# Optimization experiments

Measured on AMD Instinct MI355X. Metric: run time of the kernel, lower is better.

## Reference

```python
import jax, jax.numpy as jnp
import numpy as np

NEG_SLOPE = 0.2

def gat_conv(x, edge_index, W, a_src, a_dst, bias, heads, channels):
    # PyG GATConv (add_self_loops=False, dropout off in eval)
    N = x.shape[0]
    h = (x @ W).reshape(N, heads, channels)               # [N,H,C]
    src, dst = edge_index[0], edge_index[1]
    e_src = jnp.einsum('nhc,hc->nh', h, a_src)            # [N,H]
    e_dst = jnp.einsum('nhc,hc->nh', h, a_dst)
    e = jax.nn.leaky_relu(e_src[src] + e_dst[dst], NEG_SLOPE)  # [E,H]
    # softmax over incoming edges of each destination node
    m = jax.ops.segment_max(e, dst, num_segments=N)       # [N,H]
    ex = jnp.exp(e - m[dst])
    s = jax.ops.segment_sum(ex, dst, num_segments=N)
    alpha = ex / (s[dst] + 1e-16)                         # [E,H]
    msg = h[src] * alpha[:, :, None]                      # [E,H,C]
    out = jax.ops.segment_sum(msg, dst, num_segments=N)   # [N,H,C]
    return out.reshape(N, heads * channels) + bias


def setup_inputs() -> dict:
    key = jax.random.key(0)
    ks = jax.random.split(key, 12)
    N, E, SED, HID, H, F_OUT = 20000, 320000, 768, 128, 4, 128
    return {
        'x': jax.random.normal(ks[0], (N, SED), jnp.float32),
        'edge_index': jax.random.randint(ks[1], (2, E), 0, N, jnp.int32),
        'sentence_embedding': jax.random.normal(ks[2], (SED,), jnp.float32),
        'W1': jax.random.normal(ks[3], (2 * SED, H * HID), jnp.float32) * 0.02,
        'a1_src': jax.random.normal(ks[4], (H, HID), jnp.float32) * 0.1,
        'a1_dst': jax.random.normal(ks[5], (H, HID), jnp.float32) * 0.1,
        'b1': jax.random.normal(ks[6], (H * HID,), jnp.float32) * 0.02,
        'W2': jax.random.normal(ks[7], (H * HID, F_OUT), jnp.float32) * 0.02,
        'a2_src': jax.random.normal(ks[8], (1, F_OUT), jnp.float32) * 0.1,
        'a2_dst': jax.random.normal(ks[9], (1, F_OUT), jnp.float32) * 0.1,
        'b2': jax.random.normal(ks[10], (F_OUT,), jnp.float32) * 0.02,
    }


def reference(x, edge_index, sentence_embedding, W1, a1_src, a1_dst, b1, W2, a2_src, a2_dst, b2):
    N = x.shape[0]
    sent = jnp.broadcast_to(sentence_embedding[None, :], (N, sentence_embedding.shape[0]))
    h = jnp.concatenate([x, sent], axis=1)                # [N, 2*SED]
    h = gat_conv(h, edge_index, W1, a1_src, a1_dst, b1, heads=4, channels=128)
    h = jax.nn.elu(h)
    out = gat_conv(h, edge_index, W2, a2_src, a2_dst, b2, heads=1, channels=128)
    return out
```

## Files before the change

kernel.cpp:

```cpp
#include <hip/hip_runtime.h>
#include <cstdint>
#include <cstddef>

#define NSLOPE 0.2f
#define CAP 96

typedef __attribute__((ext_vector_type(8))) short bf16x8;
typedef __attribute__((ext_vector_type(4))) float f32x4;
typedef __attribute__((ext_vector_type(2))) float f32x2;
typedef unsigned short ushort_t;

__device__ inline ushort_t f2bf(float f) {
    union { float f; unsigned u; } v; v.f = f;
    unsigned u = v.u;
    unsigned r = (u + 0x7fffu + ((u >> 16) & 1u)) >> 16;
    return (ushort_t)r;
}
__device__ inline f32x2 unpack2(unsigned u) {
    union { unsigned u; float f; } lo, hi;
    lo.u = u << 16;
    hi.u = u & 0xffff0000u;
    f32x2 r; r.x = lo.f; r.y = hi.f;
    return r;
}
__device__ inline float leaky(float v) { return (v > 0.f) ? v : NSLOPE * v; }
__device__ inline float sel4(float4 q, bool b1, bool b2) {
    return b2 ? (b1 ? q.w : q.z) : (b1 ? q.y : q.x);
}

__global__ __launch_bounds__(256) void prep_scatter_kernel(
    const float* __restrict__ x, ushort_t* __restrict__ x_bf16, size_t nx,
    const float* __restrict__ W1, ushort_t* __restrict__ W1T,
    const float* __restrict__ W2, ushort_t* __restrict__ W2T,
    const float* __restrict__ sent, float* __restrict__ svec,
    const int* __restrict__ ei, int E,
    int* __restrict__ cnt, int* __restrict__ bucket, int nbCast)
{
    __shared__ float tile[32][33];
    int bid = blockIdx.x;
    int tid = threadIdx.x;
    if (bid < 384) {
        int k0 = (bid % 24) * 32, n0 = (bid / 24) * 32;
        int tx = tid & 31, ty = tid >> 5;
#pragma unroll
        for (int i = 0; i < 4; ++i)
            tile[ty + i * 8][tx] = W1[(size_t)(k0 + ty + i * 8) * 512 + n0 + tx];
        __syncthreads();
#pragma unroll
        for (int i = 0; i < 4; ++i)
            W1T[(size_t)(n0 + ty + i * 8) * 768 + k0 + tx] = f2bf(tile[tx][ty + i * 8]);
        return;
    }
    bid -= 384;
    if (bid < 64) {
        int k0 = (bid % 16) * 32, n0 = (bid / 16) * 32;
        int tx = tid & 31, ty = tid >> 5;
#pragma unroll
        for (int i = 0; i < 4; ++i)
            tile[ty + i * 8][tx] = W2[(size_t)(k0 + ty + i * 8) * 128 + n0 + tx];
        __syncthreads();
#pragma unroll
        for (int i = 0; i < 4; ++i)
            W2T[(size_t)(n0 + ty + i * 8) * 512 + k0 + tx] = f2bf(tile[tx][ty + i * 8]);
        return;
    }
    bid -= 64;
    if (bid < 32) {
        int cb = bid & 1, kb = bid >> 1;
        int c = cb * 256 + tid;
        int k0 = kb * 48;
        float acc = 0.f;
#pragma unroll 8
        for (int k = k0; k < k0 + 48; ++k)
            acc += sent[k] * W1[(size_t)(768 + k) * 512 + c];
        atomicAdd(&svec[c], acc);
        return;
    }
    bid -= 32;
    if (bid < nbCast) {
        size_t i = ((size_t)bid * 256 + tid) * 8;
        if (i < nx) {
            float4 v0 = *(const float4*)(x + i);
            float4 v1 = *(const float4*)(x + i + 4);
            ushort_t r[8] = { f2bf(v0.x), f2bf(v0.y), f2bf(v0.z), f2bf(v0.w),
                              f2bf(v1.x), f2bf(v1.y), f2bf(v1.z), f2bf(v1.w) };
            *(uint4*)(x_bf16 + i) = *(uint4*)r;
        }
        return;
    }
    bid -= nbCast;
    {
        int e = bid * 256 + tid;
        if (e < E) {
            int d = ei[E + e];
            int slot = atomicAdd(&cnt[d], 1);
            if (slot < CAP) bucket[d * CAP + slot] = ei[e];
        }
    }
}

__device__ inline void async_copy16(const void* g, void* l) {
    __builtin_amdgcn_global_load_lds(
        (const __attribute__((address_space(1))) unsigned int*)g,
        (__attribute__((address_space(3))) unsigned int*)l, 16, 0, 0);
}

__global__ __launch_bounds__(256) void mfma_gemm_kernel(
    const ushort_t* __restrict__ A,
    const ushort_t* __restrict__ BT,
    const float* __restrict__ bias,
    ushort_t* __restrict__ Cb,
    const float* __restrict__ asrc,
    const float* __restrict__ adst,
    float* __restrict__ e_src,
    float* __restrict__ e_dst,
    int eStride,
    int M, int K, int Nc)
{
    __shared__ __align__(16) ushort_t lA[4][64 * 32];
    __shared__ __align__(16) ushort_t lB[4][128 * 32];
    __shared__ float e_lds[64][2][2];
    const int tid = threadIdx.x;
    const int wave = tid >> 6;
    const int lane = tid & 63;

    const int hh = blockIdx.y * gridDim.x + blockIdx.x;
    const int xcd = hh & 7;
    const int slot = hh >> 3;
    const int by = xcd + 8 * (slot / gridDim.x);
    const int bx = slot % gridDim.x;

    const int col0 = bx * 128;
    const int row0 = by * 64;
    const int wm = (wave & 1) * 32;
    const int wn = (wave >> 1) * 64;
    const int q = lane >> 4;
    const int ml = lane & 15;

    f32x4 acc[2][4] = {};

    const int rA = tid >> 2;
    const int gA = (tid & 3) ^ ((rA >> 1) & 3);
    int rowS[2], gS[2];
#pragma unroll
    for (int i = 0; i < 2; ++i) {
        int p = wave * 128 + i * 64 + lane;
        int r = p >> 2, s = p & 3;
        rowS[i] = r;
        gS[i] = s ^ ((r >> 1) & 3);
    }

    auto stage = [&](int k0, int buf) {
        {
            int ga = min(row0 + rA, M - 1);
            async_copy16(A + (size_t)ga * K + k0 + gA * 8,
                         &lA[buf][(size_t)(wave * 64) * 8]);
        }
#pragma unroll
        for (int i = 0; i < 2; ++i) {
            int pbs = wave * 128 + i * 64;
            async_copy16(BT + (size_t)(col0 + rowS[i]) * K + k0 + gS[i] * 8,
                         &lB[buf][(size_t)pbs * 8]);
        }
    };

    const int nt = K >> 5;
    stage(0, 0);
    if (nt > 2) {
        stage(32, 1);
        stage(64, 2);
        asm volatile("s_waitcnt vmcnt(6)\n\ts_barrier" ::: "memory");
    } else if (nt > 1) {
        stage(32, 1);
        asm volatile("s_waitcnt vmcnt(3)\n\ts_barrier" ::: "memory");
    } else {
        asm volatile("s_waitcnt vmcnt(0)\n\ts_barrier" ::: "memory");
    }

    for (int t = 0; t < nt; ++t) {
        const int pb = t & 3;
        if (t + 3 < nt) stage((t + 3) << 5, (t + 3) & 3);
        bf16x8 af[2], bfr[4];
#pragma unroll
        for (int tt = 0; tt < 2; ++tt) {
            int m = wm + tt * 16 + ml;
            af[tt] = *(const bf16x8*)&lA[pb][(size_t)(m * 4 + (q ^ ((m >> 1) & 3))) * 8];
        }
#pragma unroll
        for (int tt = 0; tt < 4; ++tt) {
            int n = wn + tt * 16 + ml;
            bfr[tt] = *(const bf16x8*)&lB[pb][(size_t)(n * 4 + (q ^ ((n >> 1) & 3))) * 8];
        }
#pragma unroll
        for (int tm = 0; tm < 2; ++tm)
#pragma unroll
            for (int tn = 0; tn < 4; ++tn)
                acc[tm][tn] = __builtin_amdgcn_mfma_f32_16x16x32_bf16(
                    af[tm], bfr[tn], acc[tm][tn], 0, 0, 0);
        if (t + 3 < nt)
            asm volatile("s_waitcnt vmcnt(6) lgkmcnt(0)\n\ts_barrier" ::: "memory");
        else if (t + 2 < nt)
            asm volatile("s_waitcnt vmcnt(3) lgkmcnt(0)\n\ts_barrier" ::: "memory");
        else if (t + 1 < nt)
            asm volatile("s_waitcnt vmcnt(0) lgkmcnt(0)\n\ts_barrier" ::: "memory");
    }

    float es_acc[2][4] = {};
    float ed_acc[2][4] = {};
#pragma unroll
    for (int tm = 0; tm < 2; ++tm) {
        int rbase = row0 + wm + tm * 16 + q * 4;
#pragma unroll
        for (int tn = 0; tn < 4; ++tn) {
            int col = col0 + wn + tn * 16 + ml;
            float bb = bias ? bias[col] : 0.f;
            float av = asrc[col];
            float dv = adst[col];
#pragma unroll
            for (int r = 0; r < 4; ++r) {
                int row = rbase + r;
                float val = acc[tm][tn][r] + bb;
                if (row < M)
                    Cb[(size_t)row * Nc + col] = f2bf(val);
                es_acc[tm][r] += val * av;
                ed_acc[tm][r] += val * dv;
            }
        }
    }
    const int colhalf = wave >> 1;
#pragma unroll
    for (int tm = 0; tm < 2; ++tm) {
#pragma unroll
        for (int r = 0; r < 4; ++r) {
            float es = es_acc[tm][r], ed2 = ed_acc[tm][r];
#pragma unroll
            for (int st = 1; st < 16; st <<= 1) {
                es += __shfl_xor(es, st);
                ed2 += __shfl_xor(ed2, st);
            }
            if (ml == 0) {
                int rl = wm + tm * 16 + q * 4 + r;
                e_lds[rl][colhalf][0] = es;
                e_lds[rl][colhalf][1] = ed2;
            }
        }
    }
    __syncthreads();
    if (tid < 64) {
        int row = row0 + tid;
        if (row < M) {
            float es = e_lds[tid][0][0] + e_lds[tid][1][0];
            float ed2 = e_lds[tid][0][1] + e_lds[tid][1][1];
            e_src[(size_t)row * eStride + bx] = es;
            e_dst[(size_t)row * eStride + bx] = ed2;
        }
    }
}

__global__ __launch_bounds__(256) void gather1_kernel(
    const ushort_t* __restrict__ h1b, const float* __restrict__ e_src,
    const float* __restrict__ e_dst, const int* __restrict__ cnt,
    const int* __restrict__ bucket, const float* __restrict__ bias,
    ushort_t* __restrict__ outb, int N)
{
    const int lane = threadIdx.x & 63;
    const int wid0 = blockIdx.x * 4 + (threadIdx.x >> 6);
    const int nw = gridDim.x * 4;

    const int h = lane >> 4;
    const bool b1 = (h & 1), b2 = (h & 2);
    const ushort_t* hp = h1b + lane * 8;
    const int c = lane * 8;
    float bias0 = bias[c],     bias1 = bias[c + 1], bias2 = bias[c + 2],
          bias3 = bias[c + 3], bias4 = bias[c + 4], bias5 = bias[c + 5],
          bias6 = bias[c + 6], bias7 = bias[c + 7];

    for (int node = __builtin_amdgcn_readfirstlane(wid0); node < N;
         node = __builtin_amdgcn_readfirstlane(node + nw)) {
        int deg = cnt[node];
        if (deg > CAP) deg = CAP;
        int beg = node * CAP, end = beg + deg;
        float4 ed = *(const float4*)&e_dst[node * 4];
        float edh = sel4(ed, b1, b2);

        f32x2 acc[4] = {};
        float s = 0.f;

        int j = beg;
        const int nb = deg >> 2;

        int4 ia, ib;
        float4 qa0, qa1, qa2, qa3, qb0, qb1, qb2, qb3;
        uint4 ua0, ua1, ua2, ua3, ub0, ub1, ub2, ub3;

        auto load4 = [&](int jj, int4& ix,
                         float4& q0, float4& q1, float4& q2, float4& q3,
                         uint4& u0, uint4& u1, uint4& u2, uint4& u3) {
            ix.x = bucket[jj];     ix.y = bucket[jj + 1];
            ix.z = bucket[jj + 2]; ix.w = bucket[jj + 3];
            q0 = *(const float4*)&e_src[ix.x * 4];
            q1 = *(const float4*)&e_src[ix.y * 4];
            q2 = *(const float4*)&e_src[ix.z * 4];
            q3 = *(const float4*)&e_src[ix.w * 4];
            u0 = *(const uint4*)&hp[(size_t)ix.x * 512];
            u1 = *(const uint4*)&hp[(size_t)ix.y * 512];
            u2 = *(const uint4*)&hp[(size_t)ix.z * 512];
            u3 = *(const uint4*)&hp[(size_t)ix.w * 512];
        };
        auto cons4 = [&](const float4& q0, const float4& q1,
                         const float4& q2, const float4& q3,
                         const uint4& u0, const uint4& u1,
                         const uint4& u2, const uint4& u3) {
            float w0 = __expf(leaky(sel4(q0, b1, b2) + edh));
            float w1 = __expf(leaky(sel4(q1, b1, b2) + edh));
            float w2 = __expf(leaky(sel4(q2, b1, b2) + edh));
            float w3 = __expf(leaky(sel4(q3, b1, b2) + edh));
            s += (w0 + w1) + (w2 + w3);
            f32x2 wv;
            wv.x = w0; wv.y = w0;
            acc[0] += unpack2(u0.x) * wv; acc[1] += unpack2(u0.y) * wv;
            acc[2] += unpack2(u0.z) * wv; acc[3] += unpack2(u0.w) * wv;
            wv.x = w1; wv.y = w1;
            acc[0] += unpack2(u1.x) * wv; acc[1] += unpack2(u1.y) * wv;
            acc[2] += unpack2(u1.z) * wv; acc[3] += unpack2(u1.w) * wv;
            wv.x = w2; wv.y = w2;
            acc[0] += unpack2(u2.x) * wv; acc[1] += unpack2(u2.y) * wv;
            acc[2] += unpack2(u2.z) * wv; acc[3] += unpack2(u2.w) * wv;
            wv.x = w3; wv.y = w3;
            acc[0] += unpack2(u3.x) * wv; acc[1] += unpack2(u3.y) * wv;
            acc[2] += unpack2(u3.z) * wv; acc[3] += unpack2(u3.w) * wv;
        };

        if (nb > 0) {
            load4(j, ia, qa0, qa1, qa2, qa3, ua0, ua1, ua2, ua3); j += 4;
            int b = 1;
            for (; b + 1 < nb; b += 2) {
                load4(j, ib, qb0, qb1, qb2, qb3, ub0, ub1, ub2, ub3); j += 4;
                cons4(qa0, qa1, qa2, qa3, ua0, ua1, ua2, ua3);
                load4(j, ia, qa0, qa1, qa2, qa3, ua0, ua1, ua2, ua3); j += 4;
                cons4(qb0, qb1, qb2, qb3, ub0, ub1, ub2, ub3);
            }
            if (b < nb) {
                load4(j, ib, qb0, qb1, qb2, qb3, ub0, ub1, ub2, ub3); j += 4;
                cons4(qa0, qa1, qa2, qa3, ua0, ua1, ua2, ua3);
                cons4(qb0, qb1, qb2, qb3, ub0, ub1, ub2, ub3);
            } else {
                cons4(qa0, qa1, qa2, qa3, ua0, ua1, ua2, ua3);
            }
        }
        for (; j < end; ++j) {
            int s0 = bucket[j];
            float4 q0 = *(const float4*)&e_src[s0 * 4];
            float w0 = __expf(leaky(sel4(q0, b1, b2) + edh));
            s += w0;
            uint4 u0 = *(const uint4*)&hp[(size_t)s0 * 512];
            f32x2 wv; wv.x = w0; wv.y = w0;
            acc[0] += unpack2(u0.x) * wv; acc[1] += unpack2(u0.y) * wv;
            acc[2] += unpack2(u0.z) * wv; acc[3] += unpack2(u0.w) * wv;
        }
        float rs = 1.f / (s + 1e-16f);
        ushort_t o[8];
        float r0, r1;
        r0 = acc[0].x * rs + bias0; r1 = acc[0].y * rs + bias1;
        r0 = (r0 > 0.f) ? r0 : (__expf(r0) - 1.f);
        r1 = (r1 > 0.f) ? r1 : (__expf(r1) - 1.f);
        o[0] = f2bf(r0); o[1] = f2bf(r1);
        r0 = acc[1].x * rs + bias2; r1 = acc[1].y * rs + bias3;
        r0 = (r0 > 0.f) ? r0 : (__expf(r0) - 1.f);
        r1 = (r1 > 0.f) ? r1 : (__expf(r1) - 1.f);
        o[2] = f2bf(r0); o[3] = f2bf(r1);
        r0 = acc[2].x * rs + bias4; r1 = acc[2].y * rs + bias5;
        r0 = (r0 > 0.f) ? r0 : (__expf(r0) - 1.f);
        r1 = (r1 > 0.f) ? r1 : (__expf(r1) - 1.f);
        o[4] = f2bf(r0); o[5] = f2bf(r1);
        r0 = acc[3].x * rs + bias6; r1 = acc[3].y * rs + bias7;
        r0 = (r0 > 0.f) ? r0 : (__expf(r0) - 1.f);
        r1 = (r1 > 0.f) ? r1 : (__expf(r1) - 1.f);
        o[6] = f2bf(r0); o[7] = f2bf(r1);
        *(uint4*)&outb[(size_t)node * 512 + c] = *(uint4*)o;
    }
}

__global__ __launch_bounds__(256) void gather2_kernel(
    const ushort_t* __restrict__ h2b, const float* __restrict__ e_src,
    const float* __restrict__ e_dst, const int* __restrict__ cnt,
    const int* __restrict__ bucket, const float* __restrict__ bias,
    float* __restrict__ out, int N)
{
    const int lane = threadIdx.x & 63;
    const int wid0 = blockIdx.x * 4 + (threadIdx.x >> 6);
    const int nw = gridDim.x * 4;

    const ushort_t* hp = h2b + lane * 2;
    float biasA = bias[lane * 2], biasB = bias[lane * 2 + 1];

    for (int node = __builtin_amdgcn_readfirstlane(wid0); node < N;
         node = __builtin_amdgcn_readfirstlane(node + nw)) {
        int deg = cnt[node];
        if (deg > CAP) deg = CAP;
        int beg = node * CAP, end = beg + deg;
        float ed = e_dst[node];

        f32x2 acc = { 0.f, 0.f };
        float s = 0.f;

        int j = beg;
        const int nb = deg >> 2;

        int4 ia, ib;
        float fa0, fa1, fa2, fa3, fb0, fb1, fb2, fb3;
        unsigned ua0, ua1, ua2, ua3, ub0, ub1, ub2, ub3;

        auto load4 = [&](int jj, int4& ix,
                         float& f0, float& f1, float& f2, float& f3,
                         unsigned& u0, unsigned& u1, unsigned& u2, unsigned& u3) {
            ix.x = bucket[jj];     ix.y = bucket[jj + 1];
            ix.z = bucket[jj + 2]; ix.w = bucket[jj + 3];
            f0 = e_src[ix.x]; f1 = e_src[ix.y];
            f2 = e_src[ix.z]; f3 = e_src[ix.w];
            u0 = *(const unsigned*)&hp[(size_t)ix.x * 128];
            u1 = *(const unsigned*)&hp[(size_t)ix.y * 128];
            u2 = *(const unsigned*)&hp[(size_t)ix.z * 128];
            u3 = *(const unsigned*)&hp[(size_t)ix.w * 128];
        };
        auto cons4 = [&](float f0, float f1, float f2, float f3,
                         unsigned u0, unsigned u1, unsigned u2, unsigned u3) {
            float w0 = __expf(leaky(f0 + ed));
            float w1 = __expf(leaky(f1 + ed));
            float w2 = __expf(leaky(f2 + ed));
            float w3 = __expf(leaky(f3 + ed));
            s += (w0 + w1) + (w2 + w3);
            f32x2 w0v = { w0, w0 }, w1v = { w1, w1 }, w2v = { w2, w2 }, w3v = { w3, w3 };
            acc += unpack2(u0) * w0v;
            acc += unpack2(u1) * w1v;
            acc += unpack2(u2) * w2v;
            acc += unpack2(u3) * w3v;
        };

        if (nb > 0) {
            load4(j, ia, fa0, fa1, fa2, fa3, ua0, ua1, ua2, ua3); j += 4;
            int b = 1;
            for (; b + 1 < nb; b += 2) {
                load4(j, ib, fb0, fb1, fb2, fb3, ub0, ub1, ub2, ub3); j += 4;
                cons4(fa0, fa1, fa2, fa3, ua0, ua1, ua2, ua3);
                load4(j, ia, fa0, fa1, fa2, fa3, ua0, ua1, ua2, ua3); j += 4;
                cons4(fb0, fb1, fb2, fb3, ub0, ub1, ub2, ub3);
            }
            if (b < nb) {
                load4(j, ib, fb0, fb1, fb2, fb3, ub0, ub1, ub2, ub3); j += 4;
                cons4(fa0, fa1, fa2, fa3, ua0, ua1, ua2, ua3);
                cons4(fb0, fb1, fb2, fb3, ub0, ub1, ub2, ub3);
            } else {
                cons4(fa0, fa1, fa2, fa3, ua0, ua1, ua2, ua3);
            }
        }
        for (; j < end; ++j) {
            int s0 = bucket[j];
            float w0 = __expf(leaky(e_src[s0] + ed));
            s += w0;
            unsigned u0 = *(const unsigned*)&hp[(size_t)s0 * 128];
            f32x2 w0v = { w0, w0 };
            acc += unpack2(u0) * w0v;
        }
        float rs = 1.f / (s + 1e-16f);
        float2 o = make_float2(acc.x * rs + biasA, acc.y * rs + biasB);
        *(float2*)&out[(size_t)node * 128 + lane * 2] = o;
    }
}

extern "C" void kernel_launch(void* const* d_in, const int* in_sizes, int n_in,
                              void* d_out, int out_size, void* d_ws, size_t ws_size,
                              hipStream_t stream) {
    const float* x      = (const float*)d_in[0];
    const int*   ei     = (const int*)  d_in[1];
    const float* sent   = (const float*)d_in[2];
    const float* W1     = (const float*)d_in[3];
    const float* a1_src = (const float*)d_in[4];
    const float* a1_dst = (const float*)d_in[5];
    const float* b1     = (const float*)d_in[6];
    const float* W2     = (const float*)d_in[7];
    const float* a2_src = (const float*)d_in[8];
    const float* a2_dst = (const float*)d_in[9];
    const float* b2     = (const float*)d_in[10];
    float* out = (float*)d_out;

    const int N = in_sizes[0] / 768;
    const int E = in_sizes[1] / 2;

    char* p = (char*)d_ws;
    auto carve = [&](size_t bytes) {
        char* q = p;
        p += (bytes + 255) & ~(size_t)255;
        return q;
    };
    ushort_t* h1b = (ushort_t*)carve((size_t)N * 512 * 2);
    char* shared_region = carve((size_t)N * 768 * 2);
    ushort_t* x_bf16 = (ushort_t*)shared_region;
    ushort_t* h_elu_b = (ushort_t*)shared_region;
    ushort_t* h2b = (ushort_t*)carve((size_t)N * 128 * 2);
    ushort_t* W1T = (ushort_t*)carve((size_t)512 * 768 * 2);
    ushort_t* W2T = (ushort_t*)carve((size_t)128 * 512 * 2);
    float* e_src1 = (float*)carve((size_t)N * 4 * 4);
    float* e_dst1 = (float*)carve((size_t)N * 4 * 4);
    float* e_src2 = (float*)carve((size_t)N * 4);
    float* e_dst2 = (float*)carve((size_t)N * 4);
    int*   cnt    = (int*)carve((size_t)N * 4);
    float* svec   = (float*)carve(512 * 4);
    int*   bucket = (int*)carve((size_t)N * CAP * 4);

    size_t nx = (size_t)N * 768;
    int nbCast = (int)((nx / 8 + 255) / 256);
    int nbScat = (E + 255) / 256;
    int nbPrep = 384 + 64 + 32 + nbCast + nbScat;

    size_t zero_span = (size_t)((char*)(svec + 512) - (char*)cnt);
    hipMemsetAsync(cnt, 0, zero_span, stream);

    prep_scatter_kernel<<<nbPrep, 256, 0, stream>>>(
        x, x_bf16, nx, W1, W1T, W2, W2T, sent, svec, ei, E, cnt, bucket, nbCast);

    int nyPad = (((N + 63) / 64) + 7) & ~7;

    mfma_gemm_kernel<<<dim3(4, nyPad), 256, 0, stream>>>(
        x_bf16, W1T, svec, h1b, a1_src, a1_dst, e_src1, e_dst1, 4, N, 768, 512);

    gather1_kernel<<<2048, 256, 0, stream>>>(
        h1b, e_src1, e_dst1, cnt, bucket, b1, h_elu_b, N);

    mfma_gemm_kernel<<<dim3(1, nyPad), 256, 0, stream>>>(
        h_elu_b, W2T, nullptr, h2b, a2_src, a2_dst, e_src2, e_dst2, 1, N, 512, 128);

    gather2_kernel<<<2048, 256, 0, stream>>>(
        h2b, e_src2, e_dst2, cnt, bucket, b2, out, N);
}
```

Measured before the change: 250.8 us.

## Move edge bucketing into GEMM1 grid and drop memset and atomics

The edge scatter into per-destination buckets moves out of the prep kernel and runs as extra blocks appended to the first GEMM launch, so the atomic bucketing overlaps with the matrix multiply. The hipMemsetAsync is replaced by zeroing cnt inside the prep kernel. The sentence-embedding bias is now stored as 16 partial vectors, summed per column in the GEMM prologue, instead of being accumulated with atomics. This removes one launch and the float atomics, at the cost of a redundant 16-way bias sum in every GEMM block and scatter blocks competing with GEMM blocks for CUs.

Result: no change. 253.4 us (+1.0%).

```diff
diff --git a/kernel.cpp b/kernel.cpp
--- a/kernel.cpp
+++ b/kernel.cpp
@@ -28,13 +28,12 @@
     return b2 ? (b1 ? q.w : q.z) : (b1 ? q.y : q.x);
 }
 
-__global__ __launch_bounds__(256) void prep_scatter_kernel(
+__global__ __launch_bounds__(256) void prep_kernel(
     const float* __restrict__ x, ushort_t* __restrict__ x_bf16, size_t nx,
     const float* __restrict__ W1, ushort_t* __restrict__ W1T,
     const float* __restrict__ W2, ushort_t* __restrict__ W2T,
-    const float* __restrict__ sent, float* __restrict__ svec,
-    const int* __restrict__ ei, int E,
-    int* __restrict__ cnt, int* __restrict__ bucket, int nbCast)
+    const float* __restrict__ sent, float* __restrict__ svec_part,
+    int* __restrict__ cnt, int N, int nbCast)
 {
     __shared__ float tile[32][33];
     int bid = blockIdx.x;
@@ -73,7 +72,7 @@
 #pragma unroll 8
         for (int k = k0; k < k0 + 48; ++k)
             acc += sent[k] * W1[(size_t)(768 + k) * 512 + c];
-        atomicAdd(&svec[c], acc);
+        svec_part[kb * 512 + c] = acc;
         return;
     }
     bid -= 32;
@@ -90,12 +89,8 @@
     }
     bid -= nbCast;
     {
-        int e = bid * 256 + tid;
-        if (e < E) {
-            int d = ei[E + e];
-            int slot = atomicAdd(&cnt[d], 1);
-            if (slot < CAP) bucket[d * CAP + slot] = ei[e];
-        }
+        int i = bid * 256 + tid;
+        if (i < N) cnt[i] = 0;
     }
 }
 
@@ -108,14 +103,18 @@
 __global__ __launch_bounds__(256) void mfma_gemm_kernel(
     const ushort_t* __restrict__ A,
     const ushort_t* __restrict__ BT,
-    const float* __restrict__ bias,
+    const float* __restrict__ bias_part,
+    int nPart,
     ushort_t* __restrict__ Cb,
     const float* __restrict__ asrc,
     const float* __restrict__ adst,
     float* __restrict__ e_src,
     float* __restrict__ e_dst,
     int eStride,
-    int M, int K, int Nc)
+    int M, int K, int Nc,
+    int nyReal,
+    const int* __restrict__ ei, int E,
+    int* __restrict__ cnt, int* __restrict__ bucket)
 {
     __shared__ __align__(16) ushort_t lA[4][64 * 32];
     __shared__ __align__(16) ushort_t lB[4][128 * 32];
@@ -130,12 +129,33 @@
     const int by = xcd + 8 * (slot / gridDim.x);
     const int bx = slot % gridDim.x;
 
+    if (by >= nyReal) {
+        int sid = (by - nyReal) * gridDim.x + bx;
+        int e = sid * 256 + tid;
+        if (e < E) {
+            int d = ei[E + e];
+            int s = atomicAdd(&cnt[d], 1);
+            if (s < CAP) bucket[d * CAP + s] = ei[e];
+        }
+        return;
+    }
+
     const int col0 = bx * 128;
     const int row0 = by * 64;
     const int wm = (wave & 1) * 32;
     const int wn = (wave >> 1) * 64;
     const int q = lane >> 4;
     const int ml = lane & 15;
+
+    float bb4[4];
+#pragma unroll
+    for (int tn = 0; tn < 4; ++tn) {
+        int col = col0 + wn + tn * 16 + ml;
+        float sum = 0.f;
+        for (int kb = 0; kb < nPart; ++kb)
+            sum += bias_part[kb * 512 + col];
+        bb4[tn] = sum;
+    }
 
     f32x4 acc[2][4] = {};
 
@@ -213,7 +233,7 @@
 #pragma unroll
         for (int tn = 0; tn < 4; ++tn) {
             int col = col0 + wn + tn * 16 + ml;
-            float bb = bias ? bias[col] : 0.f;
+            float bb = bb4[tn];
             float av = asrc[col];
             float dv = adst[col];
 #pragma unroll
@@ -500,35 +520,37 @@
     ushort_t* h2b = (ushort_t*)carve((size_t)N * 128 * 2);
     ushort_t* W1T = (ushort_t*)carve((size_t)512 * 768 * 2);
     ushort_t* W2T = (ushort_t*)carve((size_t)128 * 512 * 2);
+    float* svec_part = (float*)carve(16 * 512 * 4);
     float* e_src1 = (float*)carve((size_t)N * 4 * 4);
     float* e_dst1 = (float*)carve((size_t)N * 4 * 4);
     float* e_src2 = (float*)carve((size_t)N * 4);
     float* e_dst2 = (float*)carve((size_t)N * 4);
     int*   cnt    = (int*)carve((size_t)N * 4);
-    float* svec   = (float*)carve(512 * 4);
     int*   bucket = (int*)carve((size_t)N * CAP * 4);
 
     size_t nx = (size_t)N * 768;
     int nbCast = (int)((nx / 8 + 255) / 256);
+    int nbZero = (N + 255) / 256;
+    int nbPrep = 384 + 64 + 32 + nbCast + nbZero;
+
+    prep_kernel<<<nbPrep, 256, 0, stream>>>(
+        x, x_bf16, nx, W1, W1T, W2, W2T, sent, svec_part, cnt, N, nbCast);
+
+    int nyReal = (((N + 63) / 64) + 7) & ~7;
     int nbScat = (E + 255) / 256;
-    int nbPrep = 384 + 64 + 32 + nbCast + nbScat;
-
-    size_t zero_span = (size_t)((char*)(svec + 512) - (char*)cnt);
-    hipMemsetAsync(cnt, 0, zero_span, stream);
-
-    prep_scatter_kernel<<<nbPrep, 256, 0, stream>>>(
-        x, x_bf16, nx, W1, W1T, W2, W2T, sent, svec, ei, E, cnt, bucket, nbCast);
-
-    int nyPad = (((N + 63) / 64) + 7) & ~7;
-
-    mfma_gemm_kernel<<<dim3(4, nyPad), 256, 0, stream>>>(
-        x_bf16, W1T, svec, h1b, a1_src, a1_dst, e_src1, e_dst1, 4, N, 768, 512);
+    int gy1 = nyReal + (nbScat + 3) / 4;
+    gy1 = (gy1 + 7) & ~7;
+
+    mfma_gemm_kernel<<<dim3(4, gy1), 256, 0, stream>>>(
+        x_bf16, W1T, svec_part, 16, h1b, a1_src, a1_dst, e_src1, e_dst1,
+        4, N, 768, 512, nyReal, ei, E, cnt, bucket);
 
     gather1_kernel<<<2048, 256, 0, stream>>>(
         h1b, e_src1, e_dst1, cnt, bucket, b1, h_elu_b, N);
 
-    mfma_gemm_kernel<<<dim3(1, nyPad), 256, 0, stream>>>(
-        h_elu_b, W2T, nullptr, h2b, a2_src, a2_dst, e_src2, e_dst2, 1, N, 512, 128);
+    mfma_gemm_kernel<<<dim3(1, nyReal), 256, 0, stream>>>(
+        h_elu_b, W2T, nullptr, 0, h2b, a2_src, a2_dst, e_src2, e_dst2,
+        1, N, 512, 128, nyReal, nullptr, 0, nullptr, nullptr);
 
     gather2_kernel<<<2048, 256, 0, stream>>>(
         h2b, e_src2, e_dst2, cnt, bucket, b2, out, N);
```
